# Optimization experiments

Measured on AMD Instinct MI355X. Metric: run time of the kernel, lower is better.

## Reference

```python
import jax, jax.numpy as jnp
import numpy as np

N_PRED = 50000
N_GT = 2000


def _make_boxes(key, n, coord_scale=1000.0, wh_scale=100.0):
    k1, k2 = jax.random.split(key)
    xy = jax.random.uniform(k1, (n, 2), dtype=jnp.float32) * coord_scale
    wh = jax.random.uniform(k2, (n, 2), dtype=jnp.float32) * wh_scale + 1.0
    return jnp.concatenate([xy, xy + wh], axis=-1)  # xyxy


def setup_inputs() -> dict:
    key = jax.random.key(0)
    kp, kg = jax.random.split(key)
    return {
        "pred_bbox": _make_boxes(kp, N_PRED),
        "gt_bbox": _make_boxes(kg, N_GT),
    }


def _bbox_overlap(pred, gt):
    # pred: [N,4], gt: [M,4], xyxy -> IoU matrix [N,M]
    lt = jnp.maximum(pred[:, None, :2], gt[None, :, :2])  # [N,M,2]
    rb = jnp.minimum(pred[:, None, 2:], gt[None, :, 2:])  # [N,M,2]
    wh = jnp.clip(rb - lt, 0.0)
    inter = wh[..., 0] * wh[..., 1]  # [N,M]
    area_p = (pred[:, 2] - pred[:, 0]) * (pred[:, 3] - pred[:, 1])  # [N]
    area_g = (gt[:, 2] - gt[:, 0]) * (gt[:, 3] - gt[:, 1])  # [M]
    union = area_p[:, None] + area_g[None, :] - inter
    return inter / union


def reference(pred_bbox, gt_bbox):
    # OverlapCalculator.calc_overlap: detach pred, pairwise IoU, row-wise max
    iou = _bbox_overlap(jax.lax.stop_gradient(pred_bbox), gt_bbox)  # [N,M]
    max_overlap = jnp.max(iou, axis=1)          # [N]
    argmax_overlap = jnp.argmax(iou, axis=1)    # [N] int
    # forward returns (pred_bbox, gt_bbox, max, argmax) per image pair
    return (pred_bbox, gt_bbox, max_overlap, argmax_overlap)
```

## Files before the change

### kernel.cpp

```cpp
#include <hip/hip_runtime.h>


#define N_PRED 50000
#define N_GT   2000
#define NXB    32
#define NYB    16
#define NCELL  (NXB * NYB)
#define BLOCK  256
#define LPP    8
#define PPB    (BLOCK / LPP)

__device__ __forceinline__ int bin1(float v, float mn, float inv, int nb) {
    int b = (int)floorf((v - mn) * inv);
    return max(0, min(nb - 1, b));
}

__global__ __launch_bounds__(512) void build_index(
        const float4* __restrict__ gt,
        float4* __restrict__ ws_gt, unsigned short* __restrict__ ws_idx,
        int* __restrict__ ws_cell, float* __restrict__ ws_par,
        float* __restrict__ out) {
#pragma clang fp contract(off)
    __shared__ float rxm[512], rxM[512], rym[512], ryM[512], rw[512], rh[512];
    __shared__ int   hist[NCELL], scan[NCELL], cursor[NCELL];
    __shared__ float s_par[6];
    const int tid = threadIdx.x;

    float xm = 3.4e38f, xM = -3.4e38f, ym = 3.4e38f, yM = -3.4e38f;
    float w = 0.0f, h = 0.0f;
    for (int j = tid; j < N_GT; j += 512) {
        const float4 g = gt[j];
        xm = fminf(xm, g.x); xM = fmaxf(xM, g.x);
        ym = fminf(ym, g.y); yM = fmaxf(yM, g.y);
        w  = fmaxf(w, g.z - g.x);
        h  = fmaxf(h, g.w - g.y);
        ((float4*)(out + 4 * N_PRED))[j] = g;
    }
    rxm[tid] = xm; rxM[tid] = xM; rym[tid] = ym; ryM[tid] = yM;
    rw[tid] = w;   rh[tid] = h;
    __syncthreads();
    for (int s = 256; s > 0; s >>= 1) {
        if (tid < s) {
            rxm[tid] = fminf(rxm[tid], rxm[tid + s]);
            rxM[tid] = fmaxf(rxM[tid], rxM[tid + s]);
            rym[tid] = fminf(rym[tid], rym[tid + s]);
            ryM[tid] = fmaxf(ryM[tid], ryM[tid + s]);
            rw[tid]  = fmaxf(rw[tid],  rw[tid + s]);
            rh[tid]  = fmaxf(rh[tid],  rh[tid + s]);
        }
        __syncthreads();
    }
    if (tid == 0) {
        s_par[0] = rxm[0];
        s_par[1] = (float)NXB / fmaxf(rxM[0] - rxm[0], 1e-20f);
        s_par[2] = rym[0];
        s_par[3] = (float)NYB / fmaxf(ryM[0] - rym[0], 1e-20f);
        s_par[4] = rw[0];
        s_par[5] = rh[0];
        for (int k = 0; k < 6; ++k) ws_par[k] = s_par[k];
    }
    hist[tid] = 0;
    __syncthreads();
    const float xmin = s_par[0], invx = s_par[1];
    const float ymin = s_par[2], invy = s_par[3];

    for (int j = tid; j < N_GT; j += 512) {
        const float4 g = gt[j];
        const int c = bin1(g.x, xmin, invx, NXB) * NYB +
                      bin1(g.y, ymin, invy, NYB);
        atomicAdd(&hist[c], 1);
    }
    __syncthreads();

    const int v = hist[tid];
    scan[tid] = v;
    __syncthreads();
    for (int off = 1; off < NCELL; off <<= 1) {
        const int t = (tid >= off) ? scan[tid - off] : 0;
        __syncthreads();
        scan[tid] += t;
        __syncthreads();
    }
    const int excl = scan[tid] - v;
    cursor[tid] = excl;
    ws_cell[tid] = excl;
    if (tid == NCELL - 1) ws_cell[NCELL] = scan[tid];
    __syncthreads();

    for (int j = tid; j < N_GT; j += 512) {
        const float4 g = gt[j];
        const int c = bin1(g.x, xmin, invx, NXB) * NYB +
                      bin1(g.y, ymin, invy, NYB);
        const int pos = atomicAdd(&cursor[c], 1);
        ws_gt[pos]  = g;
        ws_idx[pos] = (unsigned short)j;
    }
}

__global__ __launch_bounds__(BLOCK) void iou_max(
        const float4* __restrict__ pred,
        const float4* __restrict__ ws_gt, const unsigned short* __restrict__ ws_idx,
        const int* __restrict__ ws_cell, const float* __restrict__ ws_par,
        float* __restrict__ out) {
#pragma clang fp contract(off)
    __shared__ float4         sgt[N_GT];
    __shared__ unsigned short sidx[N_GT];
    __shared__ int            scell[NCELL + 1];

    for (int j = threadIdx.x; j < N_GT; j += BLOCK) {
        sgt[j]  = ws_gt[j];
        sidx[j] = ws_idx[j];
    }
    for (int j = threadIdx.x; j < NCELL + 1; j += BLOCK) scell[j] = ws_cell[j];
    const float xmin = ws_par[0], invx = ws_par[1];
    const float ymin = ws_par[2], invy = ws_par[3];
    const float mgw  = ws_par[4], mgh  = ws_par[5];
    __syncthreads();

    const int  pid = blockIdx.x * PPB + (int)(threadIdx.x >> 3);
    const int  sub = threadIdx.x & (LPP - 1);
    const bool act = pid < N_PRED;
    const float4 p  = pred[act ? pid : 0];
    const float  ap = (p.z - p.x) * (p.w - p.y);

    int bl = 0, bh = -1, yl = 0, yh1 = 0;
    if (act) {
        bl  = bin1(p.x - mgw - 0.5f, xmin, invx, NXB);
        bh  = bin1(p.z,              xmin, invx, NXB);
        yl  = bin1(p.y - mgh - 0.5f, ymin, invy, NYB);
        yh1 = bin1(p.w,              ymin, invy, NYB) + 1;
    }

    float best = 0.0f;
    int   bidx = 0;
    for (int b = bl; b <= bh; ++b) {
        const int rlo = scell[b * NYB + yl];
        const int rhi = scell[b * NYB + yh1];
        for (int t = rlo + sub; t < rhi; t += LPP) {
            const float4 g  = sgt[t];
            const int    oi = sidx[t];
            const float  ag = (g.z - g.x) * (g.w - g.y);
            const float  w  = fmaxf(fminf(p.z, g.z) - fmaxf(p.x, g.x), 0.0f);
            const float  h  = fmaxf(fminf(p.w, g.w) - fmaxf(p.y, g.y), 0.0f);
            const float  in = w * h;
            const float  un = (ap + ag) - in;
            const float  q  = in / un;
            if (q > best || (q == best && oi < bidx)) { best = q; bidx = oi; }
        }
    }
#pragma unroll
    for (int s = 1; s < LPP; s <<= 1) {
        const float oq = __shfl_xor(best, s);
        const int   oi = __shfl_xor(bidx, s);
        if (oq > best || (oq == best && oi < bidx)) { best = oq; bidx = oi; }
    }
    if (act && sub == 0) {
        ((float4*)out)[pid] = p;
        out[4 * N_PRED + 4 * N_GT + pid]          = best;
        out[4 * N_PRED + 4 * N_GT + N_PRED + pid] = (float)bidx;
    }
}

extern "C" void kernel_launch(void* const* d_in, const int* in_sizes, int n_in,
                              void* d_out, int out_size, void* d_ws, size_t ws_size,
                              hipStream_t stream) {
    const float4* pred = (const float4*)d_in[0];
    const float4* gt   = (const float4*)d_in[1];
    float* out = (float*)d_out;

    char* ws = (char*)d_ws;
    float4*         ws_gt   = (float4*)ws;
    unsigned short* ws_idx  = (unsigned short*)(ws + 32768);
    int*            ws_cell = (int*)(ws + 32768 + 4096);
    float*          ws_par  = (float*)(ws + 32768 + 4096 + 2304);

    build_index<<<1, 512, 0, stream>>>(gt, ws_gt, ws_idx, ws_cell, ws_par, out);

    const int gx = (N_PRED + PPB - 1) / PPB;
    iou_max<<<gx, BLOCK, 0, stream>>>(pred, ws_gt, ws_idx, ws_cell, ws_par, out);
}
```

Baseline: 79.85 us.

## Use wave shuffles in index build, amortize shared GT load over more preds

The single-block index builder now caches its GT boxes in registers and replaces the LDS tree reduction and Hillis-Steele scan with wavefront shuffle reductions and scans, cutting barriers. The IoU kernel uses 512-thread blocks that each handle two predictions per 8-lane group, so every block's shared-memory copy of all GT boxes serves four times as many predictions. It also skips the division when the intersection is zero. The trade-offs are fewer blocks, which may lower occupancy on a large GPU, and some extra branching in the inner loop.

```diff
diff --git a/kernel.cpp b/kernel.cpp
--- a/kernel.cpp
+++ b/kernel.cpp
@@ -6,9 +6,11 @@
 #define NXB    32
 #define NYB    16
 #define NCELL  (NXB * NYB)
-#define BLOCK  256
+#define BLOCK  512
 #define LPP    8
-#define PPB    (BLOCK / LPP)
+#define NGRP   (BLOCK / LPP)
+#define PPT    2
+#define PPB    (NGRP * PPT)
 
 __device__ __forceinline__ int bin1(float v, float mn, float inv, int nb) {
     int b = (int)floorf((v - mn) * inv);
@@ -21,79 +23,101 @@
         int* __restrict__ ws_cell, float* __restrict__ ws_par,
         float* __restrict__ out) {
 #pragma clang fp contract(off)
-    __shared__ float rxm[512], rxM[512], rym[512], ryM[512], rw[512], rh[512];
-    __shared__ int   hist[NCELL], scan[NCELL], cursor[NCELL];
+    __shared__ float wred[8][6];
+    __shared__ int   wsum[8];
     __shared__ float s_par[6];
-    const int tid = threadIdx.x;
-
+    __shared__ int   hist[NCELL];
+    const int tid  = threadIdx.x;
+    const int lane = tid & 63;
+    const int wv   = tid >> 6;
+
+    hist[tid] = 0;
+
+    float4 gr[4];
+    int    nloc = 0;
     float xm = 3.4e38f, xM = -3.4e38f, ym = 3.4e38f, yM = -3.4e38f;
     float w = 0.0f, h = 0.0f;
     for (int j = tid; j < N_GT; j += 512) {
         const float4 g = gt[j];
+        gr[nloc++] = g;
         xm = fminf(xm, g.x); xM = fmaxf(xM, g.x);
         ym = fminf(ym, g.y); yM = fmaxf(yM, g.y);
         w  = fmaxf(w, g.z - g.x);
         h  = fmaxf(h, g.w - g.y);
         ((float4*)(out + 4 * N_PRED))[j] = g;
     }
-    rxm[tid] = xm; rxM[tid] = xM; rym[tid] = ym; ryM[tid] = yM;
-    rw[tid] = w;   rh[tid] = h;
-    __syncthreads();
-    for (int s = 256; s > 0; s >>= 1) {
-        if (tid < s) {
-            rxm[tid] = fminf(rxm[tid], rxm[tid + s]);
-            rxM[tid] = fmaxf(rxM[tid], rxM[tid + s]);
-            rym[tid] = fminf(rym[tid], rym[tid + s]);
-            ryM[tid] = fmaxf(ryM[tid], ryM[tid + s]);
-            rw[tid]  = fmaxf(rw[tid],  rw[tid + s]);
-            rh[tid]  = fmaxf(rh[tid],  rh[tid + s]);
-        }
-        __syncthreads();
-    }
+#pragma unroll
+    for (int s = 1; s < 64; s <<= 1) {
+        xm = fminf(xm, __shfl_xor(xm, s));
+        xM = fmaxf(xM, __shfl_xor(xM, s));
+        ym = fminf(ym, __shfl_xor(ym, s));
+        yM = fmaxf(yM, __shfl_xor(yM, s));
+        w  = fmaxf(w,  __shfl_xor(w,  s));
+        h  = fmaxf(h,  __shfl_xor(h,  s));
+    }
+    if (lane == 0) {
+        wred[wv][0] = xm; wred[wv][1] = xM; wred[wv][2] = ym;
+        wred[wv][3] = yM; wred[wv][4] = w;  wred[wv][5] = h;
+    }
+    __syncthreads();
     if (tid == 0) {
-        s_par[0] = rxm[0];
-        s_par[1] = (float)NXB / fmaxf(rxM[0] - rxm[0], 1e-20f);
-        s_par[2] = rym[0];
-        s_par[3] = (float)NYB / fmaxf(ryM[0] - rym[0], 1e-20f);
-        s_par[4] = rw[0];
-        s_par[5] = rh[0];
+        float a0 = wred[0][0], a1 = wred[0][1], a2 = wred[0][2];
+        float a3 = wred[0][3], a4 = wred[0][4], a5 = wred[0][5];
+        for (int k = 1; k < 8; ++k) {
+            a0 = fminf(a0, wred[k][0]); a1 = fmaxf(a1, wred[k][1]);
+            a2 = fminf(a2, wred[k][2]); a3 = fmaxf(a3, wred[k][3]);
+            a4 = fmaxf(a4, wred[k][4]); a5 = fmaxf(a5, wred[k][5]);
+        }
+        s_par[0] = a0;
+        s_par[1] = (float)NXB / fmaxf(a1 - a0, 1e-20f);
+        s_par[2] = a2;
+        s_par[3] = (float)NYB / fmaxf(a3 - a2, 1e-20f);
+        s_par[4] = a4;
+        s_par[5] = a5;
         for (int k = 0; k < 6; ++k) ws_par[k] = s_par[k];
     }
-    hist[tid] = 0;
     __syncthreads();
     const float xmin = s_par[0], invx = s_par[1];
     const float ymin = s_par[2], invy = s_par[3];
 
-    for (int j = tid; j < N_GT; j += 512) {
-        const float4 g = gt[j];
-        const int c = bin1(g.x, xmin, invx, NXB) * NYB +
-                      bin1(g.y, ymin, invy, NYB);
-        atomicAdd(&hist[c], 1);
+    int cellr[4];
+    for (int i = 0; i < nloc; ++i) {
+        cellr[i] = bin1(gr[i].x, xmin, invx, NXB) * NYB +
+                   bin1(gr[i].y, ymin, invy, NYB);
+        atomicAdd(&hist[cellr[i]], 1);
     }
     __syncthreads();
 
     const int v = hist[tid];
-    scan[tid] = v;
-    __syncthreads();
-    for (int off = 1; off < NCELL; off <<= 1) {
-        const int t = (tid >= off) ? scan[tid - off] : 0;
-        __syncthreads();
-        scan[tid] += t;
-        __syncthreads();
-    }
-    const int excl = scan[tid] - v;
-    cursor[tid] = excl;
+    int x = v;
+#pragma unroll
+    for (int s = 1; s < 64; s <<= 1) {
+        const int t = __shfl_up(x, s);
+        if (lane >= s) x += t;
+    }
+    if (lane == 63) wsum[wv] = x;
+    __syncthreads();
+    if (wv == 0) {
+        int t = (lane < 8) ? wsum[lane] : 0;
+#pragma unroll
+        for (int s = 1; s < 8; s <<= 1) {
+            const int u = __shfl_up(t, s);
+            if (lane >= s) t += u;
+        }
+        if (lane < 8) wsum[lane] = t;
+    }
+    __syncthreads();
+    const int incl = x + (wv ? wsum[wv - 1] : 0);
+    const int excl = incl - v;
     ws_cell[tid] = excl;
-    if (tid == NCELL - 1) ws_cell[NCELL] = scan[tid];
-    __syncthreads();
-
-    for (int j = tid; j < N_GT; j += 512) {
-        const float4 g = gt[j];
-        const int c = bin1(g.x, xmin, invx, NXB) * NYB +
-                      bin1(g.y, ymin, invy, NYB);
-        const int pos = atomicAdd(&cursor[c], 1);
-        ws_gt[pos]  = g;
-        ws_idx[pos] = (unsigned short)j;
+    if (tid == NCELL - 1) ws_cell[NCELL] = incl;
+    hist[tid] = excl;
+    __syncthreads();
+
+    for (int i = 0; i < nloc; ++i) {
+        const int pos = atomicAdd(&hist[cellr[i]], 1);
+        ws_gt[pos]  = gr[i];
+        ws_idx[pos] = (unsigned short)(tid + i * 512);
     }
 }
 
@@ -117,47 +141,54 @@
     const float mgw  = ws_par[4], mgh  = ws_par[5];
     __syncthreads();
 
-    const int  pid = blockIdx.x * PPB + (int)(threadIdx.x >> 3);
-    const int  sub = threadIdx.x & (LPP - 1);
-    const bool act = pid < N_PRED;
-    const float4 p  = pred[act ? pid : 0];
-    const float  ap = (p.z - p.x) * (p.w - p.y);
-
-    int bl = 0, bh = -1, yl = 0, yh1 = 0;
-    if (act) {
-        bl  = bin1(p.x - mgw - 0.5f, xmin, invx, NXB);
-        bh  = bin1(p.z,              xmin, invx, NXB);
-        yl  = bin1(p.y - mgh - 0.5f, ymin, invy, NYB);
-        yh1 = bin1(p.w,              ymin, invy, NYB) + 1;
-    }
-
-    float best = 0.0f;
-    int   bidx = 0;
-    for (int b = bl; b <= bh; ++b) {
-        const int rlo = scell[b * NYB + yl];
-        const int rhi = scell[b * NYB + yh1];
-        for (int t = rlo + sub; t < rhi; t += LPP) {
-            const float4 g  = sgt[t];
-            const int    oi = sidx[t];
-            const float  ag = (g.z - g.x) * (g.w - g.y);
-            const float  w  = fmaxf(fminf(p.z, g.z) - fmaxf(p.x, g.x), 0.0f);
-            const float  h  = fmaxf(fminf(p.w, g.w) - fmaxf(p.y, g.y), 0.0f);
-            const float  in = w * h;
-            const float  un = (ap + ag) - in;
-            const float  q  = in / un;
-            if (q > best || (q == best && oi < bidx)) { best = q; bidx = oi; }
-        }
-    }
-#pragma unroll
-    for (int s = 1; s < LPP; s <<= 1) {
-        const float oq = __shfl_xor(best, s);
-        const int   oi = __shfl_xor(bidx, s);
-        if (oq > best || (oq == best && oi < bidx)) { best = oq; bidx = oi; }
-    }
-    if (act && sub == 0) {
-        ((float4*)out)[pid] = p;
-        out[4 * N_PRED + 4 * N_GT + pid]          = best;
-        out[4 * N_PRED + 4 * N_GT + N_PRED + pid] = (float)bidx;
+    const int grp = (int)(threadIdx.x >> 3);
+    const int sub = threadIdx.x & (LPP - 1);
+
+#pragma unroll
+    for (int k = 0; k < PPT; ++k) {
+        const int  pid = blockIdx.x * PPB + k * NGRP + grp;
+        const bool act = pid < N_PRED;
+        const float4 p  = pred[act ? pid : 0];
+        const float  ap = (p.z - p.x) * (p.w - p.y);
+
+        int bl = 0, bh = -1, yl = 0, yh1 = 0;
+        if (act) {
+            bl  = bin1(p.x - mgw - 0.5f, xmin, invx, NXB);
+            bh  = bin1(p.z,              xmin, invx, NXB);
+            yl  = bin1(p.y - mgh - 0.5f, ymin, invy, NYB);
+            yh1 = bin1(p.w,              ymin, invy, NYB) + 1;
+        }
+
+        float best = 0.0f;
+        int   bidx = 0;
+        for (int b = bl; b <= bh; ++b) {
+            const int rlo = scell[b * NYB + yl];
+            const int rhi = scell[b * NYB + yh1];
+            for (int t = rlo + sub; t < rhi; t += LPP) {
+                const float4 g  = sgt[t];
+                const int    oi = sidx[t];
+                const float  ag = (g.z - g.x) * (g.w - g.y);
+                const float  w  = fmaxf(fminf(p.z, g.z) - fmaxf(p.x, g.x), 0.0f);
+                const float  h  = fmaxf(fminf(p.w, g.w) - fmaxf(p.y, g.y), 0.0f);
+                const float  in = w * h;
+                if (in > 0.0f) {
+                    const float un = (ap + ag) - in;
+                    const float q  = in / un;
+                    if (q > best || (q == best && oi < bidx)) { best = q; bidx = oi; }
+                }
+            }
+        }
+#pragma unroll
+        for (int s = 1; s < LPP; s <<= 1) {
+            const float oq = __shfl_xor(best, s);
+            const int   oi = __shfl_xor(bidx, s);
+            if (oq > best || (oq == best && oi < bidx)) { best = oq; bidx = oi; }
+        }
+        if (act && sub == 0) {
+            ((float4*)out)[pid] = p;
+            out[4 * N_PRED + 4 * N_GT + pid]          = best;
+            out[4 * N_PRED + 4 * N_GT + N_PRED + pid] = (float)bidx;
+        }
     }
 }
 
```

Result: faster. 77.81 us (median of 2 runs) (-2.6%).
